# Optimization experiments

Hardware: AMD Instinct MI355X
Metric: run time of the kernel (lower is better)

The kernel has to match this reference:

```python
import jax, jax.numpy as jnp
import numpy as np

N = 100000      # nodes (size_src == size_dst)
E = 1_600_000   # edges, avg degree 16
IN = 128
HID = 128
OUT = 64
DROP_P = 0.5


def setup_inputs() -> dict:
    key = jax.random.key(0)
    ks = jax.random.split(key, 10)
    x = jax.random.normal(ks[0], (N, IN), dtype=jnp.float32)
    edge = jax.random.randint(ks[1], (2, E), 0, N, dtype=jnp.int32)
    # CuGraphSAGEConv: Linear(2*in_channels -> out_channels) over concat([agg, x]), with bias
    def lin_init(k, fan_in, fan_out):
        return jax.random.normal(k, (fan_in, fan_out), dtype=jnp.float32) / np.sqrt(fan_in)
    w0 = lin_init(ks[2], 2 * IN, HID); b0 = jnp.zeros((HID,), jnp.float32)
    w1 = lin_init(ks[3], 2 * HID, HID); b1 = jnp.zeros((HID,), jnp.float32)
    w2 = lin_init(ks[4], 2 * HID, HID); b2 = jnp.zeros((HID,), jnp.float32)
    lin_w = lin_init(ks[5], HID, OUT); lin_b = jnp.zeros((OUT,), jnp.float32)
    return {"x": x, "edge": edge, "w0": w0, "b0": b0, "w1": w1, "b1": b1,
            "w2": w2, "b2": b2, "lin_w": lin_w, "lin_b": lin_b,
            "size_src": N, "size_dst": N}


def _mean_agg(h, src, dst, n):
    # mean over incoming neighbors: agg[i] = mean_{(s->i) in E} h[s]
    msg = jnp.take(h, src, axis=0)                      # [E, d]
    s = jax.ops.segment_sum(msg, dst, num_segments=n)   # [n, d]
    deg = jax.ops.segment_sum(jnp.ones((src.shape[0],), h.dtype), dst, num_segments=n)
    return s / jnp.maximum(deg, 1.0)[:, None]


def _sage_layer(h, src, dst, n_dst, w, b, drop_key):
    agg = _mean_agg(h, src, dst, h.shape[0])            # [n, d]
    z = jnp.concatenate([agg, h], axis=-1) @ w + b      # [n, out]
    z = z[:n_dst]
    z = jax.nn.relu(z)
    keep = jax.random.bernoulli(drop_key, 1.0 - DROP_P, z.shape)
    return jnp.where(keep, z / (1.0 - DROP_P), 0.0)


def reference(x, edge, w0, b0, w1, b1, w2, b2, lin_w, lin_b, size_src, size_dst):
    src, dst = edge[0], edge[1]
    dkey = jax.random.key(42)
    h = x
    for i, (w, b) in enumerate([(w0, b0), (w1, b1), (w2, b2)]):
        h = _sage_layer(h, src, dst, size_dst, w, b, jax.random.fold_in(dkey, i))
    return h @ lin_w + lin_b
```

## Files before the change

kernel.cpp:

```cpp
#include <hip/hip_runtime.h>
#include <stdint.h>

#define NN 100000
#define NE 1600000
#define NFLAT 12800000u
#define XRANGE 12500
#define XCHUNKS 782
#define GBLK 782
#define MAXDEG 64
#define FILLB (8 * XCHUNKS)
#define CVTXB 12500
#define CVTWB 416
#define LDSW 136

typedef _Float16 f16;
typedef __attribute__((ext_vector_type(2))) _Float16 f16x2;
typedef __attribute__((ext_vector_type(4))) _Float16 f16x4;
typedef __attribute__((ext_vector_type(8))) _Float16 f16x8;
typedef __attribute__((ext_vector_type(4))) float f32x4;

__device__ __forceinline__ uint32_t rotl32(uint32_t x, int r) {
  return __builtin_amdgcn_alignbit(x, x, (32 - r) & 31);
}

__device__ __forceinline__ void tf2x32(uint32_t k0, uint32_t k1,
                                       uint32_t x0, uint32_t x1,
                                       uint32_t &o0, uint32_t &o1) {
  uint32_t ks2 = k0 ^ k1 ^ 0x1BD11BDAu;
#define TF_R(r) { x0 += x1; x1 = rotl32(x1, r); x1 ^= x0; }
  x0 += k0; x1 += k1;
  TF_R(13) TF_R(15) TF_R(26) TF_R(6)
  x0 += k1;  x1 += ks2 + 1u;
  TF_R(17) TF_R(29) TF_R(16) TF_R(24)
  x0 += ks2; x1 += k0 + 2u;
  TF_R(13) TF_R(15) TF_R(26) TF_R(6)
  x0 += k0;  x1 += k1 + 3u;
  TF_R(17) TF_R(29) TF_R(16) TF_R(24)
  x0 += k1;  x1 += ks2 + 4u;
  TF_R(13) TF_R(15) TF_R(26) TF_R(6)
  x0 += ks2; x1 += k0 + 5u;
#undef TF_R
  o0 = x0; o1 = x1;
}

static void tf2x32_host(uint32_t k0, uint32_t k1, uint32_t x0, uint32_t x1,
                        uint32_t *o0, uint32_t *o1) {
  uint32_t ks2 = k0 ^ k1 ^ 0x1BD11BDAu;
#define TF_R(r) { x0 += x1; x1 = (x1 << (r)) | (x1 >> (32 - (r))); x1 ^= x0; }
  x0 += k0; x1 += k1;
  TF_R(13) TF_R(15) TF_R(26) TF_R(6)
  x0 += k1;  x1 += ks2 + 1u;
  TF_R(17) TF_R(29) TF_R(16) TF_R(24)
  x0 += ks2; x1 += k0 + 2u;
  TF_R(13) TF_R(15) TF_R(26) TF_R(6)
  x0 += k0;  x1 += k1 + 3u;
  TF_R(17) TF_R(29) TF_R(16) TF_R(24)
  x0 += k1;  x1 += ks2 + 4u;
  TF_R(13) TF_R(15) TF_R(26) TF_R(6)
  x0 += ks2; x1 += k0 + 5u;
#undef TF_R
  *o0 = x0; *o1 = x1;
}

__global__ __launch_bounds__(256) void prep_kernel(
    const int *__restrict__ src, const int *__restrict__ dst,
    int *__restrict__ cursor, int *__restrict__ col2,
    const float *__restrict__ x, f16 *__restrict__ xh,
    const float *__restrict__ w0, const float *__restrict__ w1,
    const float *__restrict__ w2, const float *__restrict__ lw,
    f16 *__restrict__ Wk0, f16 *__restrict__ Wk1, f16 *__restrict__ Wk2,
    f16 *__restrict__ WkL) {
  const int bid = blockIdx.x;
  const int tid = threadIdx.x;
  if (bid < FILLB) {
    int xr = bid & 7;
    int chunk = bid >> 3;
    int lo = xr * XRANGE, hi = lo + XRANGE;
    int base = chunk * 2048 + tid;
#pragma unroll
    for (int t = 0; t < 8; ++t) {
      int e = base + t * 256;
      if (e < NE) {
        int d = dst[e];
        if (d >= lo && d < hi) {
          int p = atomicAdd(&cursor[d], 1);
          if (p < MAXDEG) col2[d * MAXDEG + p] = src[e];
        }
      }
    }
  } else if (bid < FILLB + CVTXB) {
    uint32_t i = (uint32_t)(bid - FILLB) * 1024u + (uint32_t)tid * 4u;
    float4 v = *(const float4 *)(x + i);
    f16x4 o;
    o[0] = (f16)v.x; o[1] = (f16)v.y; o[2] = (f16)v.z; o[3] = (f16)v.w;
    *(f16x4 *)(xh + i) = o;
  } else {
    int t = (bid - FILLB - CVTXB) * 256 + tid;
    if (t < 3 * 32768) {
      int wi = t >> 15, r = t & 32767;
      int k = r >> 7, c = r & 127;
      const float *w = (wi == 0) ? w0 : ((wi == 1) ? w1 : w2);
      f16 *o = (wi == 0) ? Wk0 : ((wi == 1) ? Wk1 : Wk2);
      o[c * 256 + k] = (f16)w[r];
    } else {
      int r = t - 3 * 32768;
      int k = r >> 6, c = r & 63;
      WkL[c * 128 + k] = (f16)lw[r];
    }
  }
}

__global__ __launch_bounds__(256) void agg_kernel(const f16 *__restrict__ h,
                                                  const int *__restrict__ deg,
                                                  const int *__restrict__ col2,
                                                  f16 *__restrict__ agg,
                                                  uint32_t *__restrict__ mrow,
                                                  uint32_t mk0, uint32_t mk1) {
  int wid = threadIdx.x >> 6;
  int lane = threadIdx.x & 63;
  int n = (blockIdx.x & 7) * XRANGE + (blockIdx.x >> 3) * 4 + wid;

  {
    uint32_t j0 = (uint32_t)n * 128u + (uint32_t)lane;
    uint32_t o0, o1, p0, p1;
    tf2x32(mk0, mk1, 0u, j0, o0, o1);
    tf2x32(mk0, mk1, 0u, j0 + 64u, p0, p1);
    unsigned long long blo = __ballot((int)(o0 ^ o1) >= 0);
    unsigned long long bhi = __ballot((int)(p0 ^ p1) >= 0);
    if (lane == 0) {
      uint4 mv;
      mv.x = (uint32_t)blo; mv.y = (uint32_t)(blo >> 32);
      mv.z = (uint32_t)bhi; mv.w = (uint32_t)(bhi >> 32);
      *(uint4 *)(mrow + (size_t)n * 4) = mv;
    }
  }

  const int beg = n * MAXDEG;
  int d = min(deg[n], MAXDEG);
  const int q4 = lane >> 4;
  const int r = lane & 15;
  float s0 = 0.f, s1 = 0.f, s2 = 0.f, s3 = 0.f;
  float s4 = 0.f, s5 = 0.f, s6 = 0.f, s7 = 0.f;
  int i = 0;
  for (; i + 16 <= d; i += 16) {
    int c0 = col2[beg + i + q4];
    int c1 = col2[beg + i + 4 + q4];
    int c2 = col2[beg + i + 8 + q4];
    int c3 = col2[beg + i + 12 + q4];
    f16x8 v0 = ((const f16x8 *)(h + (size_t)c0 * 128))[r];
    f16x8 v1 = ((const f16x8 *)(h + (size_t)c1 * 128))[r];
    f16x8 v2 = ((const f16x8 *)(h + (size_t)c2 * 128))[r];
    f16x8 v3 = ((const f16x8 *)(h + (size_t)c3 * 128))[r];
    s0 += (float)v0[0] + (float)v1[0] + (float)v2[0] + (float)v3[0];
    s1 += (float)v0[1] + (float)v1[1] + (float)v2[1] + (float)v3[1];
    s2 += (float)v0[2] + (float)v1[2] + (float)v2[2] + (float)v3[2];
    s3 += (float)v0[3] + (float)v1[3] + (float)v2[3] + (float)v3[3];
    s4 += (float)v0[4] + (float)v1[4] + (float)v2[4] + (float)v3[4];
    s5 += (float)v0[5] + (float)v1[5] + (float)v2[5] + (float)v3[5];
    s6 += (float)v0[6] + (float)v1[6] + (float)v2[6] + (float)v3[6];
    s7 += (float)v0[7] + (float)v1[7] + (float)v2[7] + (float)v3[7];
  }
  for (; i + 8 <= d; i += 8) {
    int c0 = col2[beg + i + q4];
    int c1 = col2[beg + i + 4 + q4];
    f16x8 v0 = ((const f16x8 *)(h + (size_t)c0 * 128))[r];
    f16x8 v1 = ((const f16x8 *)(h + (size_t)c1 * 128))[r];
    s0 += (float)v0[0] + (float)v1[0];
    s1 += (float)v0[1] + (float)v1[1];
    s2 += (float)v0[2] + (float)v1[2];
    s3 += (float)v0[3] + (float)v1[3];
    s4 += (float)v0[4] + (float)v1[4];
    s5 += (float)v0[5] + (float)v1[5];
    s6 += (float)v0[6] + (float)v1[6];
    s7 += (float)v0[7] + (float)v1[7];
  }
  for (; i + 4 <= d; i += 4) {
    int c = col2[beg + i + q4];
    f16x8 v = ((const f16x8 *)(h + (size_t)c * 128))[r];
    s0 += (float)v[0]; s1 += (float)v[1];
    s2 += (float)v[2]; s3 += (float)v[3];
    s4 += (float)v[4]; s5 += (float)v[5];
    s6 += (float)v[6]; s7 += (float)v[7];
  }
  if (i < d && q4 < d - i) {
    int c = col2[beg + i + q4];
    f16x8 v = ((const f16x8 *)(h + (size_t)c * 128))[r];
    s0 += (float)v[0]; s1 += (float)v[1];
    s2 += (float)v[2]; s3 += (float)v[3];
    s4 += (float)v[4]; s5 += (float)v[5];
    s6 += (float)v[6]; s7 += (float)v[7];
  }
  s0 += __shfl_xor(s0, 16); s0 += __shfl_xor(s0, 32);
  s1 += __shfl_xor(s1, 16); s1 += __shfl_xor(s1, 32);
  s2 += __shfl_xor(s2, 16); s2 += __shfl_xor(s2, 32);
  s3 += __shfl_xor(s3, 16); s3 += __shfl_xor(s3, 32);
  s4 += __shfl_xor(s4, 16); s4 += __shfl_xor(s4, 32);
  s5 += __shfl_xor(s5, 16); s5 += __shfl_xor(s5, 32);
  s6 += __shfl_xor(s6, 16); s6 += __shfl_xor(s6, 32);
  s7 += __shfl_xor(s7, 16); s7 += __shfl_xor(s7, 32);
  if (q4 == 0) {
    float inv = 1.0f / (float)max(d, 1);
    f16x8 o;
    o[0] = (f16)(s0 * inv); o[1] = (f16)(s1 * inv);
    o[2] = (f16)(s2 * inv); o[3] = (f16)(s3 * inv);
    o[4] = (f16)(s4 * inv); o[5] = (f16)(s5 * inv);
    o[6] = (f16)(s6 * inv); o[7] = (f16)(s7 * inv);
    ((f16x8 *)(agg + (size_t)n * 128))[r] = o;
  }
}

template <int FINAL>
__global__ __launch_bounds__(256) void sage_gemm_f16(
    const f16 *__restrict__ agg, const f16 *__restrict__ hin,
    const f16 *__restrict__ Wk, const float *__restrict__ bias,
    const uint32_t *__restrict__ mask, f16 *__restrict__ hout,
    const f16 *__restrict__ WkL, const float *__restrict__ lb,
    float *__restrict__ outp) {
  extern __shared__ char smem[];
  f16 (*hl)[LDSW] = (f16(*)[LDSW])smem;
  const int tid = threadIdx.x;
  const int lane = tid & 63;
  const int wv = tid >> 6;
  const int blk_row0 = blockIdx.x * 128;
  const int kg = (lane >> 4) * 8;
  const int col_lo = lane & 15;

  f16x8 Bf[2][8];
#pragma unroll
  for (int t = 0; t < 2; ++t) {
    const int colb = wv * 32 + t * 16 + col_lo;
#pragma unroll
    for (int ks = 0; ks < 8; ++ks)
      Bf[t][ks] = *(const f16x8 *)(Wk + (size_t)colb * 256 + ks * 32 + kg);
  }
  const float bv0 = bias[wv * 32 + col_lo];
  const float bv1 = bias[wv * 32 + 16 + col_lo];

#pragma unroll 2
  for (int s = 0; s < 8; ++s) {
    const int row0 = blk_row0 + s * 16;
    const int ar = row0 + col_lo;
    const bool rowok = ar < NN;
    f16x8 Af[8];
#pragma unroll
    for (int ks = 0; ks < 8; ++ks) {
      const f16 *asrc = (ks < 4)
                            ? (agg + (size_t)ar * 128 + ks * 32 + kg)
                            : (hin + (size_t)ar * 128 + (ks - 4) * 32 + kg);
      Af[ks] = rowok ? *(const f16x8 *)asrc : (f16x8){};
    }
    f32x4 acc0 = {0.f, 0.f, 0.f, 0.f}, acc1 = {0.f, 0.f, 0.f, 0.f};
#pragma unroll
    for (int ks = 0; ks < 8; ++ks) {
      acc0 = __builtin_amdgcn_mfma_f32_16x16x32_f16(Af[ks], Bf[0][ks], acc0, 0, 0, 0);
      acc1 = __builtin_amdgcn_mfma_f32_16x16x32_f16(Af[ks], Bf[1][ks], acc1, 0, 0, 0);
    }
    const int rbase = row0 + (lane >> 4) * 4;
    const int c0 = wv * 32 + col_lo;
#pragma unroll
    for (int r = 0; r < 4; ++r) {
      const int row = rbase + r;
      if (row < NN) {
        uint32_t mw = mask[(size_t)row * 4 + wv];
        float z0 = acc0[r] + bv0;
        float z1 = acc1[r] + bv1;
        z0 = (z0 > 0.f && ((mw >> col_lo) & 1u)) ? z0 * 2.f : 0.f;
        z1 = (z1 > 0.f && ((mw >> (16 + col_lo)) & 1u)) ? z1 * 2.f : 0.f;
        if constexpr (FINAL) {
          const int lr = row - blk_row0;
          hl[lr][c0] = (f16)z0;
          hl[lr][c0 + 16] = (f16)z1;
        } else {
          hout[(size_t)row * 128 + c0] = (f16)z0;
          hout[(size_t)row * 128 + c0 + 16] = (f16)z1;
        }
      }
    }
  }

  if constexpr (FINAL) {
    __syncthreads();
    const int c = wv * 16 + col_lo;
    f16x8 Bf2[4];
#pragma unroll
    for (int ks = 0; ks < 4; ++ks)
      Bf2[ks] = *(const f16x8 *)(WkL + (size_t)c * 128 + ks * 32 + kg);
    const float bv = lb[c];
#pragma unroll 2
    for (int s = 0; s < 8; ++s) {
      const int lr = s * 16 + col_lo;
      f32x4 acc = {0.f, 0.f, 0.f, 0.f};
#pragma unroll
      for (int ks = 0; ks < 4; ++ks) {
        f16x8 a = *(const f16x8 *)&hl[lr][ks * 32 + kg];
        acc = __builtin_amdgcn_mfma_f32_16x16x32_f16(a, Bf2[ks], acc, 0, 0, 0);
      }
      const int rbase = blk_row0 + s * 16 + (lane >> 4) * 4;
#pragma unroll
      for (int r = 0; r < 4; ++r) {
        const int row = rbase + r;
        if (row < NN) outp[(size_t)row * 64 + c] = acc[r] + bv;
      }
    }
  }
}

extern "C" void kernel_launch(void *const *d_in, const int *in_sizes, int n_in,
                              void *d_out, int out_size, void *d_ws,
                              size_t ws_size, hipStream_t stream) {
  (void)in_sizes; (void)n_in; (void)out_size; (void)ws_size;
  const float *x = (const float *)d_in[0];
  const int *edge = (const int *)d_in[1];
  const int *src = edge;
  const int *dst = edge + NE;
  const float *w0 = (const float *)d_in[2];
  const float *b0 = (const float *)d_in[3];
  const float *w1 = (const float *)d_in[4];
  const float *b1 = (const float *)d_in[5];
  const float *w2 = (const float *)d_in[6];
  const float *b2 = (const float *)d_in[7];
  const float *lw = (const float *)d_in[8];
  const float *lb = (const float *)d_in[9];
  float *out = (float *)d_out;

  char *ws = (char *)d_ws;
  f16 *xh  = (f16 *)ws; ws += (size_t)NN * 128 * 2;
  f16 *h1  = (f16 *)ws; ws += (size_t)NN * 128 * 2;
  f16 *h2  = (f16 *)ws; ws += (size_t)NN * 128 * 2;
  f16 *agg = (f16 *)ws; ws += (size_t)NN * 128 * 2;
  f16 *Wk0 = (f16 *)ws; ws += 256 * 128 * 2;
  f16 *Wk1 = (f16 *)ws; ws += 256 * 128 * 2;
  f16 *Wk2 = (f16 *)ws; ws += 256 * 128 * 2;
  f16 *WkL = (f16 *)ws; ws += 128 * 64 * 2;
  int *cursor = (int *)ws; ws += (size_t)NN * 4;
  int *col2 = (int *)ws;   ws += (size_t)NN * MAXDEG * 4;
  uint32_t *m0 = (uint32_t *)ws; ws += (size_t)(NFLAT / 32) * 4;
  uint32_t *m1 = (uint32_t *)ws; ws += (size_t)(NFLAT / 32) * 4;
  uint32_t *m2 = (uint32_t *)ws; ws += (size_t)(NFLAT / 32) * 4;

  uint32_t fk[3][2];
  for (int i = 0; i < 3; ++i)
    tf2x32_host(0u, 42u, 0u, (uint32_t)i, &fk[i][0], &fk[i][1]);

  hipMemsetAsync(cursor, 0, (size_t)NN * 4, stream);
  prep_kernel<<<FILLB + CVTXB + CVTWB, 256, 0, stream>>>(
      src, dst, cursor, col2, x, xh, w0, w1, w2, lw, Wk0, Wk1, Wk2, WkL);

  agg_kernel<<<NN / 4, 256, 0, stream>>>(xh, cursor, col2, agg, m0,
                                         fk[0][0], fk[0][1]);
  sage_gemm_f16<0><<<GBLK, 256, 0, stream>>>(agg, xh, Wk0, b0, m0, h1,
                                             nullptr, nullptr, nullptr);
  agg_kernel<<<NN / 4, 256, 0, stream>>>(h1, cursor, col2, agg, m1,
                                         fk[1][0], fk[1][1]);
  sage_gemm_f16<0><<<GBLK, 256, 0, stream>>>(agg, h1, Wk1, b1, m1, h2,
                                             nullptr, nullptr, nullptr);
  agg_kernel<<<NN / 4, 256, 0, stream>>>(h2, cursor, col2, agg, m2,
                                         fk[2][0], fk[2][1]);
  sage_gemm_f16<1><<<GBLK, 256, 128 * LDSW * 2, stream>>>(
      agg, h2, Wk2, b2, m2, nullptr, WkL, lb, out);
}
```

Measured before the change: 415.8 us.

## Fuse neighbor aggregation, dropout mask and GEMM into one per-layer kernel

Merges the gather-mean aggregation and the SAGE GEMM into a single 512-thread kernel per layer. Each block aggregates its 128 rows into swizzled LDS and keeps the dropout mask there, so the agg and mask buffers no longer round-trip through global memory and three launches are removed. The risk is that the gather phase now runs only 782 blocks of 8 waves, each wave handling 16 nodes serially, which lowers the parallelism available to hide latency on the irregular gather. Each wave now computes 16 output columns instead of 32.

Measured after the change: 475.1 us. 14.3% more time.

```diff
diff --git a/kernel.cpp b/kernel.cpp
--- a/kernel.cpp
+++ b/kernel.cpp
@@ -12,12 +12,15 @@
 #define CVTXB 12500
 #define CVTWB 416
 #define LDSW 136
+#define LDS_BYTES (128 * LDSW * 2 + 128 * 4 * 4)
 
 typedef _Float16 f16;
 typedef __attribute__((ext_vector_type(2))) _Float16 f16x2;
 typedef __attribute__((ext_vector_type(4))) _Float16 f16x4;
 typedef __attribute__((ext_vector_type(8))) _Float16 f16x8;
 typedef __attribute__((ext_vector_type(4))) float f32x4;
+
+#define SWZ(row, grp) ((((grp) ^ ((row) & 7)) << 3))
 
 __device__ __forceinline__ uint32_t rotl32(uint32_t x, int r) {
   return __builtin_amdgcn_alignbit(x, x, (32 - r) & 31);
@@ -110,196 +113,199 @@
   }
 }
 
-__global__ __launch_bounds__(256) void agg_kernel(const f16 *__restrict__ h,
-                                                  const int *__restrict__ deg,
-                                                  const int *__restrict__ col2,
-                                                  f16 *__restrict__ agg,
-                                                  uint32_t *__restrict__ mrow,
-                                                  uint32_t mk0, uint32_t mk1) {
-  int wid = threadIdx.x >> 6;
-  int lane = threadIdx.x & 63;
-  int n = (blockIdx.x & 7) * XRANGE + (blockIdx.x >> 3) * 4 + wid;
-
-  {
-    uint32_t j0 = (uint32_t)n * 128u + (uint32_t)lane;
-    uint32_t o0, o1, p0, p1;
-    tf2x32(mk0, mk1, 0u, j0, o0, o1);
-    tf2x32(mk0, mk1, 0u, j0 + 64u, p0, p1);
-    unsigned long long blo = __ballot((int)(o0 ^ o1) >= 0);
-    unsigned long long bhi = __ballot((int)(p0 ^ p1) >= 0);
-    if (lane == 0) {
-      uint4 mv;
-      mv.x = (uint32_t)blo; mv.y = (uint32_t)(blo >> 32);
-      mv.z = (uint32_t)bhi; mv.w = (uint32_t)(bhi >> 32);
-      *(uint4 *)(mrow + (size_t)n * 4) = mv;
-    }
-  }
-
-  const int beg = n * MAXDEG;
-  int d = min(deg[n], MAXDEG);
-  const int q4 = lane >> 4;
-  const int r = lane & 15;
-  float s0 = 0.f, s1 = 0.f, s2 = 0.f, s3 = 0.f;
-  float s4 = 0.f, s5 = 0.f, s6 = 0.f, s7 = 0.f;
-  int i = 0;
-  for (; i + 16 <= d; i += 16) {
-    int c0 = col2[beg + i + q4];
-    int c1 = col2[beg + i + 4 + q4];
-    int c2 = col2[beg + i + 8 + q4];
-    int c3 = col2[beg + i + 12 + q4];
-    f16x8 v0 = ((const f16x8 *)(h + (size_t)c0 * 128))[r];
-    f16x8 v1 = ((const f16x8 *)(h + (size_t)c1 * 128))[r];
-    f16x8 v2 = ((const f16x8 *)(h + (size_t)c2 * 128))[r];
-    f16x8 v3 = ((const f16x8 *)(h + (size_t)c3 * 128))[r];
-    s0 += (float)v0[0] + (float)v1[0] + (float)v2[0] + (float)v3[0];
-    s1 += (float)v0[1] + (float)v1[1] + (float)v2[1] + (float)v3[1];
-    s2 += (float)v0[2] + (float)v1[2] + (float)v2[2] + (float)v3[2];
-    s3 += (float)v0[3] + (float)v1[3] + (float)v2[3] + (float)v3[3];
-    s4 += (float)v0[4] + (float)v1[4] + (float)v2[4] + (float)v3[4];
-    s5 += (float)v0[5] + (float)v1[5] + (float)v2[5] + (float)v3[5];
-    s6 += (float)v0[6] + (float)v1[6] + (float)v2[6] + (float)v3[6];
-    s7 += (float)v0[7] + (float)v1[7] + (float)v2[7] + (float)v3[7];
-  }
-  for (; i + 8 <= d; i += 8) {
-    int c0 = col2[beg + i + q4];
-    int c1 = col2[beg + i + 4 + q4];
-    f16x8 v0 = ((const f16x8 *)(h + (size_t)c0 * 128))[r];
-    f16x8 v1 = ((const f16x8 *)(h + (size_t)c1 * 128))[r];
-    s0 += (float)v0[0] + (float)v1[0];
-    s1 += (float)v0[1] + (float)v1[1];
-    s2 += (float)v0[2] + (float)v1[2];
-    s3 += (float)v0[3] + (float)v1[3];
-    s4 += (float)v0[4] + (float)v1[4];
-    s5 += (float)v0[5] + (float)v1[5];
-    s6 += (float)v0[6] + (float)v1[6];
-    s7 += (float)v0[7] + (float)v1[7];
-  }
-  for (; i + 4 <= d; i += 4) {
-    int c = col2[beg + i + q4];
-    f16x8 v = ((const f16x8 *)(h + (size_t)c * 128))[r];
-    s0 += (float)v[0]; s1 += (float)v[1];
-    s2 += (float)v[2]; s3 += (float)v[3];
-    s4 += (float)v[4]; s5 += (float)v[5];
-    s6 += (float)v[6]; s7 += (float)v[7];
-  }
-  if (i < d && q4 < d - i) {
-    int c = col2[beg + i + q4];
-    f16x8 v = ((const f16x8 *)(h + (size_t)c * 128))[r];
-    s0 += (float)v[0]; s1 += (float)v[1];
-    s2 += (float)v[2]; s3 += (float)v[3];
-    s4 += (float)v[4]; s5 += (float)v[5];
-    s6 += (float)v[6]; s7 += (float)v[7];
-  }
-  s0 += __shfl_xor(s0, 16); s0 += __shfl_xor(s0, 32);
-  s1 += __shfl_xor(s1, 16); s1 += __shfl_xor(s1, 32);
-  s2 += __shfl_xor(s2, 16); s2 += __shfl_xor(s2, 32);
-  s3 += __shfl_xor(s3, 16); s3 += __shfl_xor(s3, 32);
-  s4 += __shfl_xor(s4, 16); s4 += __shfl_xor(s4, 32);
-  s5 += __shfl_xor(s5, 16); s5 += __shfl_xor(s5, 32);
-  s6 += __shfl_xor(s6, 16); s6 += __shfl_xor(s6, 32);
-  s7 += __shfl_xor(s7, 16); s7 += __shfl_xor(s7, 32);
-  if (q4 == 0) {
-    float inv = 1.0f / (float)max(d, 1);
-    f16x8 o;
-    o[0] = (f16)(s0 * inv); o[1] = (f16)(s1 * inv);
-    o[2] = (f16)(s2 * inv); o[3] = (f16)(s3 * inv);
-    o[4] = (f16)(s4 * inv); o[5] = (f16)(s5 * inv);
-    o[6] = (f16)(s6 * inv); o[7] = (f16)(s7 * inv);
-    ((f16x8 *)(agg + (size_t)n * 128))[r] = o;
-  }
-}
-
 template <int FINAL>
-__global__ __launch_bounds__(256) void sage_gemm_f16(
-    const f16 *__restrict__ agg, const f16 *__restrict__ hin,
-    const f16 *__restrict__ Wk, const float *__restrict__ bias,
-    const uint32_t *__restrict__ mask, f16 *__restrict__ hout,
-    const f16 *__restrict__ WkL, const float *__restrict__ lb,
-    float *__restrict__ outp) {
+__global__ __launch_bounds__(512, 6) void sage_layer(
+    const f16 *__restrict__ hin, const int *__restrict__ deg,
+    const int *__restrict__ col2, const f16 *__restrict__ Wk,
+    const float *__restrict__ bias, f16 *__restrict__ hout,
+    const f16 *__restrict__ WkL, const float *__restrict__ lbias,
+    float *__restrict__ outp, uint32_t mk0, uint32_t mk1) {
   extern __shared__ char smem[];
-  f16 (*hl)[LDSW] = (f16(*)[LDSW])smem;
+  f16 (*agl)[LDSW] = (f16(*)[LDSW])smem;
+  uint32_t *mws = (uint32_t *)(smem + 128 * LDSW * 2);
   const int tid = threadIdx.x;
   const int lane = tid & 63;
   const int wv = tid >> 6;
   const int blk_row0 = blockIdx.x * 128;
-  const int kg = (lane >> 4) * 8;
+
+  {
+    const int q4 = lane >> 4;
+    const int r = lane & 15;
+    for (int ii = 0; ii < 16; ++ii) {
+      const int ln = wv * 16 + ii;
+      const int n = blk_row0 + ln;
+      uint32_t j0 = (uint32_t)n * 128u + (uint32_t)lane;
+      uint32_t o0, o1, p0, p1;
+      tf2x32(mk0, mk1, 0u, j0, o0, o1);
+      tf2x32(mk0, mk1, 0u, j0 + 64u, p0, p1);
+      unsigned long long blo = __ballot((int)(o0 ^ o1) >= 0);
+      unsigned long long bhi = __ballot((int)(p0 ^ p1) >= 0);
+      if (lane == 0) {
+        uint4 mv;
+        mv.x = (uint32_t)blo; mv.y = (uint32_t)(blo >> 32);
+        mv.z = (uint32_t)bhi; mv.w = (uint32_t)(bhi >> 32);
+        *(uint4 *)&mws[ln * 4] = mv;
+      }
+      const int beg = n * MAXDEG;
+      int d = (n < NN) ? min(deg[n], MAXDEG) : 0;
+      float s0 = 0.f, s1 = 0.f, s2 = 0.f, s3 = 0.f;
+      float s4 = 0.f, s5 = 0.f, s6 = 0.f, s7 = 0.f;
+      int i = 0;
+      for (; i + 16 <= d; i += 16) {
+        int c0 = col2[beg + i + q4];
+        int c1 = col2[beg + i + 4 + q4];
+        int c2 = col2[beg + i + 8 + q4];
+        int c3 = col2[beg + i + 12 + q4];
+        f16x8 v0 = ((const f16x8 *)(hin + (size_t)c0 * 128))[r];
+        f16x8 v1 = ((const f16x8 *)(hin + (size_t)c1 * 128))[r];
+        f16x8 v2 = ((const f16x8 *)(hin + (size_t)c2 * 128))[r];
+        f16x8 v3 = ((const f16x8 *)(hin + (size_t)c3 * 128))[r];
+        s0 += (float)v0[0] + (float)v1[0] + (float)v2[0] + (float)v3[0];
+        s1 += (float)v0[1] + (float)v1[1] + (float)v2[1] + (float)v3[1];
+        s2 += (float)v0[2] + (float)v1[2] + (float)v2[2] + (float)v3[2];
+        s3 += (float)v0[3] + (float)v1[3] + (float)v2[3] + (float)v3[3];
+        s4 += (float)v0[4] + (float)v1[4] + (float)v2[4] + (float)v3[4];
+        s5 += (float)v0[5] + (float)v1[5] + (float)v2[5] + (float)v3[5];
+        s6 += (float)v0[6] + (float)v1[6] + (float)v2[6] + (float)v3[6];
+        s7 += (float)v0[7] + (float)v1[7] + (float)v2[7] + (float)v3[7];
+      }
+      for (; i + 8 <= d; i += 8) {
+        int c0 = col2[beg + i + q4];
+        int c1 = col2[beg + i + 4 + q4];
+        f16x8 v0 = ((const f16x8 *)(hin + (size_t)c0 * 128))[r];
+        f16x8 v1 = ((const f16x8 *)(hin + (size_t)c1 * 128))[r];
+        s0 += (float)v0[0] + (float)v1[0];
+        s1 += (float)v0[1] + (float)v1[1];
+        s2 += (float)v0[2] + (float)v1[2];
+        s3 += (float)v0[3] + (float)v1[3];
+        s4 += (float)v0[4] + (float)v1[4];
+        s5 += (float)v0[5] + (float)v1[5];
+        s6 += (float)v0[6] + (float)v1[6];
+        s7 += (float)v0[7] + (float)v1[7];
+      }
+      for (; i + 4 <= d; i += 4) {
+        int c = col2[beg + i + q4];
+        f16x8 v = ((const f16x8 *)(hin + (size_t)c * 128))[r];
+        s0 += (float)v[0]; s1 += (float)v[1];
+        s2 += (float)v[2]; s3 += (float)v[3];
+        s4 += (float)v[4]; s5 += (float)v[5];
+        s6 += (float)v[6]; s7 += (float)v[7];
+      }
+      if (i < d && q4 < d - i) {
+        int c = col2[beg + i + q4];
+        f16x8 v = ((const f16x8 *)(hin + (size_t)c * 128))[r];
+        s0 += (float)v[0]; s1 += (float)v[1];
+        s2 += (float)v[2]; s3 += (float)v[3];
+        s4 += (float)v[4]; s5 += (float)v[5];
+        s6 += (float)v[6]; s7 += (float)v[7];
+      }
+      s0 += __shfl_xor(s0, 16); s0 += __shfl_xor(s0, 32);
+      s1 += __shfl_xor(s1, 16); s1 += __shfl_xor(s1, 32);
+      s2 += __shfl_xor(s2, 16); s2 += __shfl_xor(s2, 32);
+      s3 += __shfl_xor(s3, 16); s3 += __shfl_xor(s3, 32);
+      s4 += __shfl_xor(s4, 16); s4 += __shfl_xor(s4, 32);
+      s5 += __shfl_xor(s5, 16); s5 += __shfl_xor(s5, 32);
+      s6 += __shfl_xor(s6, 16); s6 += __shfl_xor(s6, 32);
+      s7 += __shfl_xor(s7, 16); s7 += __shfl_xor(s7, 32);
+      if (q4 == 0) {
+        float inv = 1.0f / (float)max(d, 1);
+        f16x8 o;
+        o[0] = (f16)(s0 * inv); o[1] = (f16)(s1 * inv);
+        o[2] = (f16)(s2 * inv); o[3] = (f16)(s3 * inv);
+        o[4] = (f16)(s4 * inv); o[5] = (f16)(s5 * inv);
+        o[6] = (f16)(s6 * inv); o[7] = (f16)(s7 * inv);
+        *(f16x8 *)&agl[ln][SWZ(ln, r)] = o;
+      }
+    }
+  }
+  __syncthreads();
+
+  const int hi = lane >> 4;
+  const int kg = hi * 8;
   const int col_lo = lane & 15;
-
-  f16x8 Bf[2][8];
-#pragma unroll
-  for (int t = 0; t < 2; ++t) {
-    const int colb = wv * 32 + t * 16 + col_lo;
-#pragma unroll
-    for (int ks = 0; ks < 8; ++ks)
-      Bf[t][ks] = *(const f16x8 *)(Wk + (size_t)colb * 256 + ks * 32 + kg);
-  }
-  const float bv0 = bias[wv * 32 + col_lo];
-  const float bv1 = bias[wv * 32 + 16 + col_lo];
-
-#pragma unroll 2
+  const int c = wv * 16 + col_lo;
+  f16x8 Bf[8];
+#pragma unroll
+  for (int ks = 0; ks < 8; ++ks)
+    Bf[ks] = *(const f16x8 *)(Wk + (size_t)c * 256 + ks * 32 + kg);
+  const float bv = bias[c];
+  const int mwsel = wv >> 1;
+  const int sh = ((wv & 1) << 4) | col_lo;
+
+  f32x4 accAll[FINAL ? 8 : 1];
+#pragma unroll
   for (int s = 0; s < 8; ++s) {
-    const int row0 = blk_row0 + s * 16;
-    const int ar = row0 + col_lo;
+    const int ar = blk_row0 + s * 16 + col_lo;
+    const int lr = s * 16 + col_lo;
     const bool rowok = ar < NN;
     f16x8 Af[8];
 #pragma unroll
-    for (int ks = 0; ks < 8; ++ks) {
-      const f16 *asrc = (ks < 4)
-                            ? (agg + (size_t)ar * 128 + ks * 32 + kg)
-                            : (hin + (size_t)ar * 128 + (ks - 4) * 32 + kg);
-      Af[ks] = rowok ? *(const f16x8 *)asrc : (f16x8){};
-    }
-    f32x4 acc0 = {0.f, 0.f, 0.f, 0.f}, acc1 = {0.f, 0.f, 0.f, 0.f};
-#pragma unroll
-    for (int ks = 0; ks < 8; ++ks) {
-      acc0 = __builtin_amdgcn_mfma_f32_16x16x32_f16(Af[ks], Bf[0][ks], acc0, 0, 0, 0);
-      acc1 = __builtin_amdgcn_mfma_f32_16x16x32_f16(Af[ks], Bf[1][ks], acc1, 0, 0, 0);
-    }
-    const int rbase = row0 + (lane >> 4) * 4;
-    const int c0 = wv * 32 + col_lo;
-#pragma unroll
-    for (int r = 0; r < 4; ++r) {
-      const int row = rbase + r;
-      if (row < NN) {
-        uint32_t mw = mask[(size_t)row * 4 + wv];
-        float z0 = acc0[r] + bv0;
-        float z1 = acc1[r] + bv1;
-        z0 = (z0 > 0.f && ((mw >> col_lo) & 1u)) ? z0 * 2.f : 0.f;
-        z1 = (z1 > 0.f && ((mw >> (16 + col_lo)) & 1u)) ? z1 * 2.f : 0.f;
-        if constexpr (FINAL) {
-          const int lr = row - blk_row0;
-          hl[lr][c0] = (f16)z0;
-          hl[lr][c0 + 16] = (f16)z1;
-        } else {
-          hout[(size_t)row * 128 + c0] = (f16)z0;
-          hout[(size_t)row * 128 + c0 + 16] = (f16)z1;
+    for (int ks = 0; ks < 4; ++ks)
+      Af[ks] = *(const f16x8 *)&agl[lr][SWZ(lr, 4 * ks + hi)];
+#pragma unroll
+    for (int ks = 4; ks < 8; ++ks)
+      Af[ks] = rowok
+                   ? *(const f16x8 *)(hin + (size_t)ar * 128 + (ks - 4) * 32 + kg)
+                   : (f16x8){};
+    f32x4 acc = {0.f, 0.f, 0.f, 0.f};
+#pragma unroll
+    for (int ks = 0; ks < 8; ++ks)
+      acc = __builtin_amdgcn_mfma_f32_16x16x32_f16(Af[ks], Bf[ks], acc, 0, 0, 0);
+    if constexpr (!FINAL) {
+      const int rbase = blk_row0 + s * 16 + hi * 4;
+#pragma unroll
+      for (int r = 0; r < 4; ++r) {
+        const int row = rbase + r;
+        if (row < NN) {
+          uint32_t mw = mws[(row - blk_row0) * 4 + mwsel];
+          float z = acc[r] + bv;
+          z = (z > 0.f && ((mw >> sh) & 1u)) ? z * 2.f : 0.f;
+          hout[(size_t)row * 128 + c] = (f16)z;
         }
       }
+    } else {
+      accAll[s] = acc;
     }
   }
 
   if constexpr (FINAL) {
     __syncthreads();
-    const int c = wv * 16 + col_lo;
+#pragma unroll
+    for (int s = 0; s < 8; ++s) {
+      const int rb = s * 16 + hi * 4;
+#pragma unroll
+      for (int r = 0; r < 4; ++r) {
+        const int lr = rb + r;
+        uint32_t mw = mws[lr * 4 + mwsel];
+        float z = accAll[s][r] + bv;
+        z = (z > 0.f && ((mw >> sh) & 1u)) ? z * 2.f : 0.f;
+        agl[lr][SWZ(lr, c >> 3) | (c & 7)] = (f16)z;
+      }
+    }
+    __syncthreads();
+    const int cg = wv & 3;
+    const int rh = wv >> 2;
+    const int fc = cg * 16 + col_lo;
     f16x8 Bf2[4];
 #pragma unroll
     for (int ks = 0; ks < 4; ++ks)
-      Bf2[ks] = *(const f16x8 *)(WkL + (size_t)c * 128 + ks * 32 + kg);
-    const float bv = lb[c];
-#pragma unroll 2
-    for (int s = 0; s < 8; ++s) {
+      Bf2[ks] = *(const f16x8 *)(WkL + (size_t)fc * 128 + ks * 32 + kg);
+    const float fbv = lbias[fc];
+#pragma unroll
+    for (int s2 = 0; s2 < 4; ++s2) {
+      const int s = rh * 4 + s2;
       const int lr = s * 16 + col_lo;
       f32x4 acc = {0.f, 0.f, 0.f, 0.f};
 #pragma unroll
       for (int ks = 0; ks < 4; ++ks) {
-        f16x8 a = *(const f16x8 *)&hl[lr][ks * 32 + kg];
+        f16x8 a = *(const f16x8 *)&agl[lr][SWZ(lr, 4 * ks + hi)];
         acc = __builtin_amdgcn_mfma_f32_16x16x32_f16(a, Bf2[ks], acc, 0, 0, 0);
       }
-      const int rbase = blk_row0 + s * 16 + (lane >> 4) * 4;
+      const int rbase = blk_row0 + s * 16 + hi * 4;
 #pragma unroll
       for (int r = 0; r < 4; ++r) {
         const int row = rbase + r;
-        if (row < NN) outp[(size_t)row * 64 + c] = acc[r] + bv;
+        if (row < NN) outp[(size_t)row * 64 + fc] = acc[r] + fbv;
       }
     }
   }
@@ -327,16 +333,12 @@
   f16 *xh  = (f16 *)ws; ws += (size_t)NN * 128 * 2;
   f16 *h1  = (f16 *)ws; ws += (size_t)NN * 128 * 2;
   f16 *h2  = (f16 *)ws; ws += (size_t)NN * 128 * 2;
-  f16 *agg = (f16 *)ws; ws += (size_t)NN * 128 * 2;
   f16 *Wk0 = (f16 *)ws; ws += 256 * 128 * 2;
   f16 *Wk1 = (f16 *)ws; ws += 256 * 128 * 2;
   f16 *Wk2 = (f16 *)ws; ws += 256 * 128 * 2;
   f16 *WkL = (f16 *)ws; ws += 128 * 64 * 2;
   int *cursor = (int *)ws; ws += (size_t)NN * 4;
   int *col2 = (int *)ws;   ws += (size_t)NN * MAXDEG * 4;
-  uint32_t *m0 = (uint32_t *)ws; ws += (size_t)(NFLAT / 32) * 4;
-  uint32_t *m1 = (uint32_t *)ws; ws += (size_t)(NFLAT / 32) * 4;
-  uint32_t *m2 = (uint32_t *)ws; ws += (size_t)(NFLAT / 32) * 4;
 
   uint32_t fk[3][2];
   for (int i = 0; i < 3; ++i)
@@ -346,16 +348,13 @@
   prep_kernel<<<FILLB + CVTXB + CVTWB, 256, 0, stream>>>(
       src, dst, cursor, col2, x, xh, w0, w1, w2, lw, Wk0, Wk1, Wk2, WkL);
 
-  agg_kernel<<<NN / 4, 256, 0, stream>>>(xh, cursor, col2, agg, m0,
-                                         fk[0][0], fk[0][1]);
-  sage_gemm_f16<0><<<GBLK, 256, 0, stream>>>(agg, xh, Wk0, b0, m0, h1,
-                                             nullptr, nullptr, nullptr);
-  agg_kernel<<<NN / 4, 256, 0, stream>>>(h1, cursor, col2, agg, m1,
-                                         fk[1][0], fk[1][1]);
-  sage_gemm_f16<0><<<GBLK, 256, 0, stream>>>(agg, h1, Wk1, b1, m1, h2,
-                                             nullptr, nullptr, nullptr);
-  agg_kernel<<<NN / 4, 256, 0, stream>>>(h2, cursor, col2, agg, m2,
-                                         fk[2][0], fk[2][1]);
-  sage_gemm_f16<1><<<GBLK, 256, 128 * LDSW * 2, stream>>>(
-      agg, h2, Wk2, b2, m2, nullptr, WkL, lb, out);
-}
+  sage_layer<0><<<GBLK, 512, LDS_BYTES, stream>>>(
+      xh, cursor, col2, Wk0, b0, h1, nullptr, nullptr, nullptr,
+      fk[0][0], fk[0][1]);
+  sage_layer<0><<<GBLK, 512, LDS_BYTES, stream>>>(
+      h1, cursor, col2, Wk1, b1, h2, nullptr, nullptr, nullptr,
+      fk[1][0], fk[1][1]);
+  sage_layer<1><<<GBLK, 512, LDS_BYTES, stream>>>(
+      h2, cursor, col2, Wk2, b2, nullptr, WkL, lb, out,
+      fk[2][0], fk[2][1]);
+}
```
